# Performance work log

Hardware: AMD Instinct MI355X
Metric: run time of the kernel (lower is better)

The kernel has to match this reference:

```python
import jax, jax.numpy as jnp
import numpy as np
from jax import lax

B, DIM, H, W = 4, 256, 128, 128
KS, LOC, STRIDES_CFG, HEADS = 5, [2, 3], [1, 2], 8
C2 = DIM // 2
GK = HEADS * KS  # per-pixel dynamic kernel channels

def _kernel_map(ks, kstride, kloc):
    # replicates LSAMixer.generate_kernel_map_1d
    axes, strides, start = [0], [1], 1
    for loc, s in zip(kloc, kstride):
        for num in range(0, loc - start):
            axes.append(num * s + axes[-1] + strides[-1])
            strides.append(s)
        start = loc
    patch = (axes[-1] + strides[-1]) * 2 - 1
    full_axes = [-a for a in axes[:0:-1]] + axes
    full_strides = strides[:0:-1] + strides
    return full_axes, full_strides, patch

OFFS, STRDS, PATCH = _kernel_map(KS, STRIDES_CFG, LOC)
PAD = PATCH // 2

def _pw(x, w, b):
    # 1x1 conv as GEMM
    return jnp.einsum('bchw,oc->bohw', x, w) + b[None, :, None, None]

def _dw(x, w, b, ph, pw):
    # depthwise conv, torch OIHW layout with I=1
    y = lax.conv_general_dilated(x, w, (1, 1), [(ph, ph), (pw, pw)],
                                 feature_group_count=x.shape[1],
                                 dimension_numbers=('NCHW', 'OIHW', 'NCHW'))
    return y + b[None, :, None, None]

def _fsa(x, kern, groups, axis):
    # dynamic local attention: for each tap k (offset a, stride s) gather the
    # average of x over the s-wide strided window along `axis`, weight it by
    # the per-head dynamic kernel, and accumulate.
    Bx, Cx, Hx, Wx = x.shape
    gd = Cx // groups
    K = len(OFFS)
    L = x.shape[axis]
    padcfg = [(0, 0)] * 4
    padcfg[axis] = (PAD, PAD)
    xp = jnp.pad(x, padcfg)
    taps = []
    for a, s in zip(OFFS, STRDS):
        start = a if a >= 0 else a - s + 1  # window covers s pixels away from center
        acc = lax.slice_in_dim(xp, PAD + start, PAD + start + L, axis=axis)
        for d in range(1, s):
            acc = acc + lax.slice_in_dim(xp, PAD + start + d, PAD + start + d + L, axis=axis)
        taps.append(acc / s)
    t = jnp.stack(taps, 0).reshape(K, Bx, groups, gd, Hx, Wx)
    k = kern.reshape(Bx, groups, K, Hx, Wx)
    return jnp.einsum('kbgdhw,bgkhw->bgdhw', t, k).reshape(Bx, Cx, Hx, Wx)

def setup_inputs() -> dict:
    key = jax.random.key(0)
    ks = jax.random.split(key, 12)
    sc = 0.02
    f32 = jnp.float32
    return {
        'x': jax.random.normal(ks[0], (B, DIM, H, W), f32),
        'proj_in_w': jax.random.normal(ks[1], (DIM, DIM), f32) * sc,
        'proj_in_b': jnp.zeros((DIM,), f32),
        'hk_dw_w': jax.random.normal(ks[2], (C2, 1, 1, PATCH), f32) * sc,
        'hk_dw_b': jnp.zeros((C2,), f32),
        'hk_pw_w': jax.random.normal(ks[3], (GK, C2), f32) * sc,
        'hk_pw_b': jnp.zeros((GK,), f32),
        'vk_dw_w': jax.random.normal(ks[4], (C2, 1, PATCH, 1), f32) * sc,
        'vk_dw_b': jnp.zeros((C2,), f32),
        'vk_pw_w': jax.random.normal(ks[5], (GK, C2), f32) * sc,
        'vk_pw_b': jnp.zeros((GK,), f32),
        'cb_w1': jax.random.normal(ks[6], (DIM // 4, C2), f32) * sc,
        'cb_b1': jnp.zeros((DIM // 4,), f32),
        'cb_w2': jax.random.normal(ks[7], (C2, DIM // 4), f32) * sc,
        'cb_b2': jnp.zeros((C2,), f32),
        'proj_out_w': jax.random.normal(ks[8], (DIM, DIM), f32) * sc,
        'proj_out_b': jnp.zeros((DIM,), f32),
    }

def reference(x, proj_in_w, proj_in_b, hk_dw_w, hk_dw_b, hk_pw_w, hk_pw_b,
              vk_dw_w, vk_dw_b, vk_pw_w, vk_pw_b, cb_w1, cb_b1, cb_w2, cb_b2,
              proj_out_w, proj_out_b):
    Bv, _, Hv, Wv = x.shape
    h = _pw(x, proj_in_w, proj_in_b)
    x1, x2 = h[:, :C2], h[:, C2:]
    # channel branch: pw -> relu -> pw
    x_conv = _pw(jax.nn.relu(_pw(x1, cb_w1, cb_b1)), cb_w2, cb_b2)
    # horizontal dynamic kernel + fsa
    kh = jnp.tanh(_pw(_dw(x2, hk_dw_w, hk_dw_b, 0, PAD), hk_pw_w, hk_pw_b))
    attn_h = _fsa(x2, kh, HEADS, axis=3)
    # vertical dynamic kernel + fsa
    kv = jnp.tanh(_pw(_dw(attn_h, vk_dw_w, vk_dw_b, PAD, 0), vk_pw_w, vk_pw_b))
    attn = _fsa(attn_h, kv, HEADS, axis=2)
    N = Hv * Wv
    xc = x_conv.reshape(Bv, C2, N)
    at = attn.reshape(Bv, C2, N)
    # SpatialInteraction(x_conv, attn): modulates x_conv
    s_sig = jax.nn.sigmoid(jnp.einsum('bc,bcn->bn', at.mean(-1), xc) / C2)[:, None, :]
    spatial_map = (s_sig * xc).reshape(Bv, C2, Hv, Wv)
    # ChannelInteraction(x_conv, attn): modulates attn
    c_sig = jax.nn.sigmoid(jnp.einsum('bcn,bn->bc', at, xc.mean(1)) / N)[:, :, None]
    channel_map = (c_sig * at).reshape(Bv, C2, Hv, Wv)
    out = jnp.concatenate([spatial_map, channel_map], axis=1)
    return _pw(out, proj_out_w, proj_out_b)
```

## Files before the change

kernel.cpp:

```cpp
#include <hip/hip_runtime.h>
#include <hip/hip_bf16.h>
#include <math.h>

typedef __hip_bfloat16 bf16;
typedef __attribute__((ext_vector_type(8))) short short8;
typedef __attribute__((ext_vector_type(4))) float floatx4;
#define DEV __device__ __forceinline__

constexpr int BATCH = 4;
constexpr int DIM   = 256;
constexpr int C2    = 128;
constexpr int GK    = 40;
constexpr int HH    = 128;
constexpr int WW    = 128;
constexpr int NPIX  = HH * WW;
constexpr int TPB   = 256;

DEV float toF(float v) { return v; }
DEV float toF(bf16 v)  { return __bfloat162float(v); }

DEV unsigned short f2bs(float f) {
  union { bf16 h; unsigned short u; } cv;
  cv.h = __float2bfloat16(f);
  return cv.u;
}
DEV float bs2f(unsigned short u) {
  union { float f; unsigned x; } c;
  c.x = ((unsigned)u) << 16;
  return c.f;
}

template<int N>
DEV void load_f32v(const float* __restrict__ p, float* v) {
  if constexpr (N == 8) {
    const float4 a = *(const float4*)p;
    const float4 b = *(const float4*)(p + 4);
    v[0]=a.x; v[1]=a.y; v[2]=a.z; v[3]=a.w; v[4]=b.x; v[5]=b.y; v[6]=b.z; v[7]=b.w;
  } else if constexpr (N == 4) {
    const float4 a = *(const float4*)p;
    v[0]=a.x; v[1]=a.y; v[2]=a.z; v[3]=a.w;
  } else {
    const float2 a = *(const float2*)p;
    v[0]=a.x; v[1]=a.y;
  }
}
template<int N>
DEV void load_bf16v(const bf16* __restrict__ p, float* v) {
  if constexpr (N == 8) {
    const uint4 u = *(const uint4*)p;
    v[0]=bs2f(u.x & 0xffff); v[1]=bs2f(u.x >> 16);
    v[2]=bs2f(u.y & 0xffff); v[3]=bs2f(u.y >> 16);
    v[4]=bs2f(u.z & 0xffff); v[5]=bs2f(u.z >> 16);
    v[6]=bs2f(u.w & 0xffff); v[7]=bs2f(u.w >> 16);
  } else if constexpr (N == 4) {
    const uint2 u = *(const uint2*)p;
    v[0]=bs2f(u.x & 0xffff); v[1]=bs2f(u.x >> 16);
    v[2]=bs2f(u.y & 0xffff); v[3]=bs2f(u.y >> 16);
  } else {
    const unsigned u = *(const unsigned*)p;
    v[0]=bs2f(u & 0xffff); v[1]=bs2f(u >> 16);
  }
}
DEV void load8bf(const bf16* __restrict__ p, float* v) { load_bf16v<8>(p, v); }

__global__ __launch_bounds__(TPB) void prepack_kernel(
    const float* __restrict__ w0, const float* __restrict__ w1,
    const float* __restrict__ w2, const float* __restrict__ w3,
    const float* __restrict__ w4, const float* __restrict__ w5,
    short* __restrict__ dst) {
  const int i = blockIdx.x * TPB + threadIdx.x;
  if (i >= 157696) return;
  int j = i;
  float v;
  if (j < 65536) v = w0[j];
  else if ((j -= 65536) < 8192) v = w1[j];
  else if ((j -= 8192) < 8192) v = w2[j];
  else if ((j -= 8192) < 5120) v = w3[j];
  else if ((j -= 5120) < 5120) v = w4[j];
  else { j -= 5120; v = w5[j]; }
  dst[i] = (short)f2bs(v);
}

template<int K, int O, int ACT, int GATED, typename TIN, typename TOUT>
__global__ __launch_bounds__(TPB) void pw2_kernel(
    const TIN* __restrict__ in, int in_bs,
    const short* __restrict__ wbf, const float* __restrict__ bias,
    TOUT* __restrict__ out, int out_bs,
    const bf16* __restrict__ gxc, const bf16* __restrict__ gattn,
    const float* __restrict__ gs, const float* __restrict__ gc) {
  constexpr int C8   = K / 8;
  constexpr int PXT  = K / 32;
  constexpr int PG   = 64 / PXT;
  constexpr int ROWB = K * 2 + 16;
  constexpr int WO   = (O + 63) / 64;
  __shared__ char smem[64 * ROWB];

  const int p0   = blockIdx.x * 64;
  const int b    = blockIdx.y;
  const int t    = threadIdx.x;
  const int lane = t & 63, wid = t >> 6;
  const int q    = lane >> 4, i16 = lane & 15;

  {
    const int c8  = t / PG;
    const int px0 = (t % PG) * PXT;
    float vals[8][PXT];
    float svals[PXT];
    if constexpr (GATED) {
      if (c8 < C8 / 2) load_f32v<PXT>(gs + (size_t)b * NPIX + p0 + px0, svals);
    }
#pragma unroll
    for (int j = 0; j < 8; ++j) {
      const int c = c8 * 8 + j;
      float tmp[PXT];
      if constexpr (GATED) {
        if (c < C2) {
          load_bf16v<PXT>(gxc + ((size_t)b * C2 + c) * NPIX + p0 + px0, tmp);
#pragma unroll
          for (int px = 0; px < PXT; ++px) vals[j][px] = tmp[px] * svals[px];
        } else {
          const float cg = gc[b * C2 + (c - C2)];
          load_bf16v<PXT>(gattn + ((size_t)b * C2 + (c - C2)) * NPIX + p0 + px0, tmp);
#pragma unroll
          for (int px = 0; px < PXT; ++px) vals[j][px] = tmp[px] * cg;
        }
      } else {
        const TIN* src = in + ((size_t)b * in_bs + c) * NPIX + p0 + px0;
        if constexpr (sizeof(TIN) == 4) load_f32v<PXT>((const float*)src, tmp);
        else                            load_bf16v<PXT>((const bf16*)src, tmp);
#pragma unroll
        for (int px = 0; px < PXT; ++px) vals[j][px] = tmp[px];
      }
    }
#pragma unroll
    for (int px = 0; px < PXT; ++px) {
      const int p = px0 + px;
      short8 pk;
#pragma unroll
      for (int j = 0; j < 8; ++j) pk[j] = (short)f2bs(vals[j][px]);
      const int phys = c8 ^ ((p >> 3) & 7);
      *reinterpret_cast<short8*>(smem + (size_t)p * ROWB + phys * 16) = pk;
    }
  }
  __syncthreads();

  const int o_base = wid * WO * 16;
  if (o_base >= O) return;

  floatx4 acc[WO][4];
#pragma unroll
  for (int ot = 0; ot < WO; ++ot)
#pragma unroll
    for (int nt = 0; nt < 4; ++nt)
      acc[ot][nt] = (floatx4){0.f, 0.f, 0.f, 0.f};

  for (int kc = 0; kc < K / 32; ++kc) {
    short8 afrag[WO];
#pragma unroll
    for (int ot = 0; ot < WO; ++ot) {
      int o = o_base + ot * 16 + i16;
      if (o >= O) o = O - 1;
      afrag[ot] = *reinterpret_cast<const short8*>(wbf + (size_t)o * K + kc * 32 + q * 8);
    }
    short8 bfrag[4];
#pragma unroll
    for (int nt = 0; nt < 4; ++nt) {
      const int n = nt * 16 + i16;
      const int phys = (kc * 4 + q) ^ ((n >> 3) & 7);
      bfrag[nt] = *reinterpret_cast<const short8*>(smem + (size_t)n * ROWB + phys * 16);
    }
#pragma unroll
    for (int ot = 0; ot < WO; ++ot)
#pragma unroll
      for (int nt = 0; nt < 4; ++nt)
        acc[ot][nt] = __builtin_amdgcn_mfma_f32_16x16x32_bf16(
            afrag[ot], bfrag[nt], acc[ot][nt], 0, 0, 0);
  }

#pragma unroll
  for (int ot = 0; ot < WO; ++ot) {
#pragma unroll
    for (int reg = 0; reg < 4; ++reg) {
      const int o = o_base + ot * 16 + q * 4 + reg;
      if (o < O) {
        const float bv = bias[o];
#pragma unroll
        for (int nt = 0; nt < 4; ++nt) {
          float v = acc[ot][nt][reg] + bv;
          if (ACT == 1) v = fmaxf(v, 0.0f);
          if (ACT == 2) v = tanhf(v);
          TOUT* dst = out + ((size_t)b * out_bs + o) * NPIX + p0 + nt * 16 + i16;
          if constexpr (sizeof(TOUT) == 4) *dst = v;
          else *dst = __float2bfloat16(v);
        }
      }
    }
  }
}

__global__ __launch_bounds__(TPB) void pwfused_kernel(
    const float* __restrict__ x,
    const short* __restrict__ w_pi, const float* __restrict__ pib,
    const short* __restrict__ w_cb1, const float* __restrict__ cbb1,
    const short* __restrict__ w_cb2, const float* __restrict__ cbb2,
    float* __restrict__ x2out, bf16* __restrict__ xconv) {
  constexpr int ROWB  = 256 * 2 + 16;
  constexpr int HROWB = 128 * 2 + 16;
  constexpr int TROWB = 64 * 2 + 16;
  __shared__ char smem[64 * ROWB];
  __shared__ char hbuf[64 * HROWB];
  __shared__ char tbuf[64 * TROWB];

  const int p0   = blockIdx.x * 64;
  const int b    = blockIdx.y;
  const int t    = threadIdx.x;
  const int lane = t & 63, wid = t >> 6;
  const int q    = lane >> 4, i16 = lane & 15;

  {
    const int c8  = t / 8;
    const int px0 = (t % 8) * 8;
    float vals[8][8];
#pragma unroll
    for (int j = 0; j < 8; ++j) {
      const int c = c8 * 8 + j;
      load_f32v<8>(x + ((size_t)b * DIM + c) * NPIX + p0 + px0, vals[j]);
    }
#pragma unroll
    for (int px = 0; px < 8; ++px) {
      const int p = px0 + px;
      short8 pk;
#pragma unroll
      for (int j = 0; j < 8; ++j) pk[j] = (short)f2bs(vals[j][px]);
      const int phys = c8 ^ ((p >> 3) & 7);
      *reinterpret_cast<short8*>(smem + (size_t)p * ROWB + phys * 16) = pk;
    }
  }
  __syncthreads();

  const int o_base = wid * 64;
  {
    floatx4 acc[4][4];
#pragma unroll
    for (int ot = 0; ot < 4; ++ot)
#pragma unroll
      for (int nt = 0; nt < 4; ++nt)
        acc[ot][nt] = (floatx4){0.f, 0.f, 0.f, 0.f};

    for (int kc = 0; kc < 8; ++kc) {
      short8 afrag[4];
#pragma unroll
      for (int ot = 0; ot < 4; ++ot) {
        const int o = o_base + ot * 16 + i16;
        afrag[ot] = *reinterpret_cast<const short8*>(w_pi + (size_t)o * 256 + kc * 32 + q * 8);
      }
      short8 bfrag[4];
#pragma unroll
      for (int nt = 0; nt < 4; ++nt) {
        const int n = nt * 16 + i16;
        const int phys = (kc * 4 + q) ^ ((n >> 3) & 7);
        bfrag[nt] = *reinterpret_cast<const short8*>(smem + (size_t)n * ROWB + phys * 16);
      }
#pragma unroll
      for (int ot = 0; ot < 4; ++ot)
#pragma unroll
        for (int nt = 0; nt < 4; ++nt)
          acc[ot][nt] = __builtin_amdgcn_mfma_f32_16x16x32_bf16(
              afrag[ot], bfrag[nt], acc[ot][nt], 0, 0, 0);
    }

#pragma unroll
    for (int ot = 0; ot < 4; ++ot) {
      const int ch0 = o_base + ot * 16 + q * 4;
      if (ch0 >= C2) {
#pragma unroll
        for (int reg = 0; reg < 4; ++reg) {
          const int o = ch0 + reg;
          const float bv = pib[o];
#pragma unroll
          for (int nt = 0; nt < 4; ++nt)
            x2out[((size_t)b * C2 + (o - C2)) * NPIX + p0 + nt * 16 + i16] =
                acc[ot][nt][reg] + bv;
        }
      } else {
        float bv4[4];
#pragma unroll
        for (int reg = 0; reg < 4; ++reg) bv4[reg] = pib[ch0 + reg];
#pragma unroll
        for (int nt = 0; nt < 4; ++nt) {
          const int px = nt * 16 + i16;
          ushort4 pk;
          pk.x = f2bs(acc[ot][nt][0] + bv4[0]);
          pk.y = f2bs(acc[ot][nt][1] + bv4[1]);
          pk.z = f2bs(acc[ot][nt][2] + bv4[2]);
          pk.w = f2bs(acc[ot][nt][3] + bv4[3]);
          const int phys = (ch0 >> 3) ^ ((px >> 3) & 7);
          *reinterpret_cast<ushort4*>(hbuf + (size_t)px * HROWB + phys * 16 +
                                      (ch0 & 7) * 2) = pk;
        }
      }
    }
  }
  __syncthreads();

  {
    floatx4 acc2[4];
#pragma unroll
    for (int nt = 0; nt < 4; ++nt) acc2[nt] = (floatx4){0.f, 0.f, 0.f, 0.f};
    const int o2b = wid * 16;
    for (int kc = 0; kc < 4; ++kc) {
      const short8 afrag = *reinterpret_cast<const short8*>(
          w_cb1 + (size_t)(o2b + i16) * 128 + kc * 32 + q * 8);
      short8 bfrag[4];
#pragma unroll
      for (int nt = 0; nt < 4; ++nt) {
        const int n = nt * 16 + i16;
        const int phys = (kc * 4 + q) ^ ((n >> 3) & 7);
        bfrag[nt] = *reinterpret_cast<const short8*>(hbuf + (size_t)n * HROWB + phys * 16);
      }
#pragma unroll
      for (int nt = 0; nt < 4; ++nt)
        acc2[nt] = __builtin_amdgcn_mfma_f32_16x16x32_bf16(afrag, bfrag[nt], acc2[nt], 0, 0, 0);
    }
    const int ch0 = o2b + q * 4;
    float bv4[4];
#pragma unroll
    for (int reg = 0; reg < 4; ++reg) bv4[reg] = cbb1[ch0 + reg];
#pragma unroll
    for (int nt = 0; nt < 4; ++nt) {
      const int px = nt * 16 + i16;
      ushort4 pk;
      pk.x = f2bs(fmaxf(acc2[nt][0] + bv4[0], 0.f));
      pk.y = f2bs(fmaxf(acc2[nt][1] + bv4[1], 0.f));
      pk.z = f2bs(fmaxf(acc2[nt][2] + bv4[2], 0.f));
      pk.w = f2bs(fmaxf(acc2[nt][3] + bv4[3], 0.f));
      const int phys = (ch0 >> 3) ^ ((px >> 3) & 7);
      *reinterpret_cast<ushort4*>(tbuf + (size_t)px * TROWB + phys * 16 +
                                  (ch0 & 7) * 2) = pk;
    }
  }
  __syncthreads();

  {
    floatx4 acc3[2][4];
#pragma unroll
    for (int ot = 0; ot < 2; ++ot)
#pragma unroll
      for (int nt = 0; nt < 4; ++nt) acc3[ot][nt] = (floatx4){0.f, 0.f, 0.f, 0.f};
    const int o3b = wid * 32;
    for (int kc = 0; kc < 2; ++kc) {
      short8 afrag[2];
#pragma unroll
      for (int ot = 0; ot < 2; ++ot)
        afrag[ot] = *reinterpret_cast<const short8*>(
            w_cb2 + (size_t)(o3b + ot * 16 + i16) * 64 + kc * 32 + q * 8);
      short8 bfrag[4];
#pragma unroll
      for (int nt = 0; nt < 4; ++nt) {
        const int n = nt * 16 + i16;
        const int phys = (kc * 4 + q) ^ ((n >> 3) & 7);
        bfrag[nt] = *reinterpret_cast<const short8*>(tbuf + (size_t)n * TROWB + phys * 16);
      }
#pragma unroll
      for (int ot = 0; ot < 2; ++ot)
#pragma unroll
        for (int nt = 0; nt < 4; ++nt)
          acc3[ot][nt] = __builtin_amdgcn_mfma_f32_16x16x32_bf16(
              afrag[ot], bfrag[nt], acc3[ot][nt], 0, 0, 0);
    }
#pragma unroll
    for (int ot = 0; ot < 2; ++ot) {
#pragma unroll
      for (int reg = 0; reg < 4; ++reg) {
        const int o = o3b + ot * 16 + q * 4 + reg;
        const float bv = cbb2[o];
#pragma unroll
        for (int nt = 0; nt < 4; ++nt)
          xconv[((size_t)b * C2 + o) * NPIX + p0 + nt * 16 + i16] =
              __float2bfloat16(acc3[ot][nt][reg] + bv);
      }
    }
  }
}

__global__ __launch_bounds__(TPB) void dwh2_kernel(
    const float* __restrict__ in, int in_bs,
    const float* __restrict__ w7, const float* __restrict__ bias,
    bf16* __restrict__ out) {
  const int g  = blockIdx.x * TPB + threadIdx.x;
  const int w8 = g & 15;
  const int hp = (g >> 4) & (HH - 1);
  const int c  = (g >> 11) & (C2 - 1);
  const int b  = g >> 18;
  const float* xr = in + ((size_t)b * in_bs + c) * NPIX + hp * WW;
  const int px0 = w8 * 8;
  float xs[14];
  if (w8 > 0) { const float4 L = *(const float4*)(xr + px0 - 4); xs[0]=L.y; xs[1]=L.z; xs[2]=L.w; }
  else { xs[0]=xs[1]=xs[2]=0.f; }
  { const float4 a = *(const float4*)(xr + px0);
    const float4 bq = *(const float4*)(xr + px0 + 4);
    xs[3]=a.x; xs[4]=a.y; xs[5]=a.z; xs[6]=a.w;
    xs[7]=bq.x; xs[8]=bq.y; xs[9]=bq.z; xs[10]=bq.w; }
  if (w8 < 15) { const float4 R = *(const float4*)(xr + px0 + 8); xs[11]=R.x; xs[12]=R.y; xs[13]=R.z; }
  else { xs[11]=xs[12]=xs[13]=0.f; }
  float wv[7];
#pragma unroll
  for (int j = 0; j < 7; ++j) wv[j] = w7[c * 7 + j];
  const float bv = bias[c];
  short8 o;
#pragma unroll
  for (int i = 0; i < 8; ++i) {
    float a = bv;
#pragma unroll
    for (int j = 0; j < 7; ++j) a = fmaf(wv[j], xs[i + j], a);
    o[i] = (short)f2bs(a);
  }
  *reinterpret_cast<short8*>(out + ((size_t)(b * C2 + c)) * NPIX + hp * WW + px0) = o;
}

__global__ __launch_bounds__(TPB) void dwv2_kernel(
    const bf16* __restrict__ in,
    const float* __restrict__ w7, const float* __restrict__ bias,
    bf16* __restrict__ out) {
  const int g  = blockIdx.x * TPB + threadIdx.x;
  const int w8 = g & 15;
  const int hp = (g >> 4) & (HH - 1);
  const int c  = (g >> 11) & (C2 - 1);
  const int b  = g >> 18;
  const int px0 = w8 * 8;
  const bf16* base = in + ((size_t)(b * C2 + c)) * NPIX + px0;
  float r[7][8];
#pragma unroll
  for (int j = 0; j < 7; ++j) {
    const int hq = hp - 3 + j;
    if (hq >= 0 && hq < HH) load8bf(base + (size_t)hq * WW, r[j]);
    else
#pragma unroll
      for (int i = 0; i < 8; ++i) r[j][i] = 0.f;
  }
  float wv[7];
#pragma unroll
  for (int j = 0; j < 7; ++j) wv[j] = w7[c * 7 + j];
  const float bv = bias[c];
  short8 o;
#pragma unroll
  for (int i = 0; i < 8; ++i) {
    float a = bv;
#pragma unroll
    for (int j = 0; j < 7; ++j) a = fmaf(wv[j], r[j][i], a);
    o[i] = (short)f2bs(a);
  }
  *reinterpret_cast<short8*>(out + ((size_t)(b * C2 + c)) * NPIX + hp * WW + px0) = o;
}

__global__ __launch_bounds__(TPB) void fsah2_kernel(
    const float* __restrict__ x, int x_bs,
    const bf16* __restrict__ kern, bf16* __restrict__ out) {
  const int g  = blockIdx.x * TPB + threadIdx.x;
  const int w8 = g & 15;
  const int hp = (g >> 4) & (HH - 1);
  const int c  = (g >> 11) & (C2 - 1);
  const int b  = g >> 18;
  const float* xr = x + ((size_t)b * x_bs + c) * NPIX + hp * WW;
  const int px0 = w8 * 8;
  float xs[14];
  if (w8 > 0) { const float4 L = *(const float4*)(xr + px0 - 4); xs[0]=L.y; xs[1]=L.z; xs[2]=L.w; }
  else { xs[0]=xs[1]=xs[2]=0.f; }
  { const float4 a = *(const float4*)(xr + px0);
    const float4 bq = *(const float4*)(xr + px0 + 4);
    xs[3]=a.x; xs[4]=a.y; xs[5]=a.z; xs[6]=a.w;
    xs[7]=bq.x; xs[8]=bq.y; xs[9]=bq.z; xs[10]=bq.w; }
  if (w8 < 15) { const float4 R = *(const float4*)(xr + px0 + 8); xs[11]=R.x; xs[12]=R.y; xs[13]=R.z; }
  else { xs[11]=xs[12]=xs[13]=0.f; }
  float k[5][8];
  const bf16* kr = kern + ((size_t)b * GK + (c >> 4) * 5) * NPIX + hp * WW + px0;
#pragma unroll
  for (int tp = 0; tp < 5; ++tp) load8bf(kr + (size_t)tp * NPIX, k[tp]);
  short8 o;
#pragma unroll
  for (int i = 0; i < 8; ++i) {
    float a = 0.5f * (xs[i] + xs[i + 1]) * k[0][i];
    a = fmaf(xs[i + 2], k[1][i], a);
    a = fmaf(xs[i + 3], k[2][i], a);
    a = fmaf(xs[i + 4], k[3][i], a);
    a = fmaf(0.5f * (xs[i + 5] + xs[i + 6]), k[4][i], a);
    o[i] = (short)f2bs(a);
  }
  *reinterpret_cast<short8*>(out + ((size_t)(b * C2 + c)) * NPIX + hp * WW + px0) = o;
}

__global__ __launch_bounds__(TPB) void fsav2_kernel(
    const bf16* __restrict__ x,
    const bf16* __restrict__ kern, bf16* __restrict__ out) {
  const int g  = blockIdx.x * TPB + threadIdx.x;
  const int w8 = g & 15;
  const int hp = (g >> 4) & (HH - 1);
  const int c  = (g >> 11) & (C2 - 1);
  const int b  = g >> 18;
  const int px0 = w8 * 8;
  const bf16* base = x + ((size_t)(b * C2 + c)) * NPIX + px0;
  float r[7][8];
#pragma unroll
  for (int j = 0; j < 7; ++j) {
    const int hq = hp - 3 + j;
    if (hq >= 0 && hq < HH) load8bf(base + (size_t)hq * WW, r[j]);
    else
#pragma unroll
      for (int i = 0; i < 8; ++i) r[j][i] = 0.f;
  }
  float k[5][8];
  const bf16* kr = kern + ((size_t)b * GK + (c >> 4) * 5) * NPIX + hp * WW + px0;
#pragma unroll
  for (int tp = 0; tp < 5; ++tp) load8bf(kr + (size_t)tp * NPIX, k[tp]);
  short8 o;
#pragma unroll
  for (int i = 0; i < 8; ++i) {
    float a = 0.5f * (r[0][i] + r[1][i]) * k[0][i];
    a = fmaf(r[2][i], k[1][i], a);
    a = fmaf(r[3][i], k[2][i], a);
    a = fmaf(r[4][i], k[3][i], a);
    a = fmaf(0.5f * (r[5][i] + r[6][i]), k[4][i], a);
    o[i] = (short)f2bs(a);
  }
  *reinterpret_cast<short8*>(out + ((size_t)(b * C2 + c)) * NPIX + hp * WW + px0) = o;
}

DEV float block_reduce_sum(float v) {
#pragma unroll
  for (int off = 32; off > 0; off >>= 1) v += __shfl_down(v, off, 64);
  __shared__ float ls[TPB / 64];
  const int lane = threadIdx.x & 63;
  const int wid  = threadIdx.x >> 6;
  if (lane == 0) ls[wid] = v;
  __syncthreads();
  float s = 0.0f;
  if (threadIdx.x == 0) {
#pragma unroll
    for (int i = 0; i < TPB / 64; ++i) s += ls[i];
  }
  return s;
}

__global__ __launch_bounds__(TPB) void mean_n_kernel(const bf16* __restrict__ in,
                                                     float* __restrict__ out) {
  const int bc = blockIdx.x;
  const bf16* r = in + (size_t)bc * NPIX;
  float s = 0.0f;
  for (int i = threadIdx.x * 8; i < NPIX; i += TPB * 8) {
    float v[8];
    load8bf(r + i, v);
#pragma unroll
    for (int j = 0; j < 8; ++j) s += v[j];
  }
  s = block_reduce_sum(s);
  if (threadIdx.x == 0) out[bc] = s * (1.0f / NPIX);
}

__global__ __launch_bounds__(TPB) void xs_kernel(const bf16* __restrict__ xc,
                                                 const float* __restrict__ at_mean,
                                                 float* __restrict__ xc_mean,
                                                 float* __restrict__ s_sig) {
  __shared__ float am[C2];
  const int b = blockIdx.y;
  if (threadIdx.x < C2) am[threadIdx.x] = at_mean[b * C2 + threadIdx.x];
  __syncthreads();
  const int p = blockIdx.x * TPB + threadIdx.x;
  const bf16* r = xc + (size_t)b * C2 * NPIX + p;
  float s = 0.0f, m = 0.0f;
#pragma unroll 4
  for (int c = 0; c < C2; ++c) {
    const float v = toF(r[(size_t)c * NPIX]);
    m += v;
    s = fmaf(am[c], v, s);
  }
  xc_mean[(size_t)b * NPIX + p] = m * (1.0f / C2);
  s_sig[(size_t)b * NPIX + p]   = 1.0f / (1.0f + expf(-s * (1.0f / C2)));
}

__global__ __launch_bounds__(TPB) void csig_kernel(const bf16* __restrict__ attn,
                                                   const float* __restrict__ xc_mean,
                                                   float* __restrict__ out) {
  const int bc = blockIdx.x;
  const int b  = bc / C2;
  const bf16* r = attn + (size_t)bc * NPIX;
  const float* m = xc_mean + (size_t)b * NPIX;
  float s = 0.0f;
  for (int i = threadIdx.x * 8; i < NPIX; i += TPB * 8) {
    float v[8], mm[8];
    load8bf(r + i, v);
    load_f32v<8>(m + i, mm);
#pragma unroll
    for (int j = 0; j < 8; ++j) s = fmaf(v[j], mm[j], s);
  }
  s = block_reduce_sum(s);
  if (threadIdx.x == 0) out[bc] = 1.0f / (1.0f + expf(-s * (1.0f / NPIX)));
}

extern "C" void kernel_launch(void* const* d_in, const int* in_sizes, int n_in,
                              void* d_out, int out_size, void* d_ws, size_t ws_size,
                              hipStream_t stream) {
  const float* x    = (const float*)d_in[0];
  const float* piw  = (const float*)d_in[1];
  const float* pib  = (const float*)d_in[2];
  const float* hkdw = (const float*)d_in[3];
  const float* hkdb = (const float*)d_in[4];
  const float* hkpw = (const float*)d_in[5];
  const float* hkpb = (const float*)d_in[6];
  const float* vkdw = (const float*)d_in[7];
  const float* vkdb = (const float*)d_in[8];
  const float* vkpw = (const float*)d_in[9];
  const float* vkpb = (const float*)d_in[10];
  const float* cbw1 = (const float*)d_in[11];
  const float* cbb1 = (const float*)d_in[12];
  const float* cbw2 = (const float*)d_in[13];
  const float* cbb2 = (const float*)d_in[14];
  const float* pow_ = (const float*)d_in[15];
  const float* pob  = (const float*)d_in[16];
  float* out = (float*)d_out;

  char* ws = (char*)d_ws;
  size_t off = 0;
  auto alloc = [&](size_t bytes) -> char* {
    char* p = ws + off;
    off += (bytes + 255) & ~(size_t)255;
    return p;
  };
  short* wpk    = (short*)alloc(157696 * 2);
  float* x2buf  = (float*)alloc((size_t)BATCH * C2  * NPIX * 4);
  bf16*  x_conv = (bf16*) alloc((size_t)BATCH * C2  * NPIX * 2);
  bf16*  dwbuf  = (bf16*) alloc((size_t)BATCH * C2  * NPIX * 2);
  bf16*  kbuf   = (bf16*) alloc((size_t)BATCH * GK  * NPIX * 2);
  bf16*  attn_h = (bf16*) alloc((size_t)BATCH * C2  * NPIX * 2);
  bf16*  attn   = (bf16*) alloc((size_t)BATCH * C2  * NPIX * 2);
  float* at_mean = (float*)alloc((size_t)BATCH * C2 * 4);
  float* xc_mean = (float*)alloc((size_t)BATCH * NPIX * 4);
  float* s_sig   = (float*)alloc((size_t)BATCH * NPIX * 4);
  float* c_sig   = (float*)alloc((size_t)BATCH * C2 * 4);

  const short* w_pi  = wpk;
  const short* w_cb1 = wpk + 65536;
  const short* w_cb2 = wpk + 73728;
  const short* w_hk  = wpk + 81920;
  const short* w_vk  = wpk + 87040;
  const short* w_po  = wpk + 92160;

  const dim3 blk(TPB);
  const dim3 gemm_grid(NPIX / 64, BATCH);
  const int PT  = NPIX / TPB;
  const int EL8 = BATCH * C2 * HH * 16 / TPB;

  prepack_kernel<<<dim3((157696 + TPB - 1) / TPB), blk, 0, stream>>>(
      piw, cbw1, cbw2, hkpw, vkpw, pow_, wpk);
  pwfused_kernel<<<gemm_grid, blk, 0, stream>>>(
      x, w_pi, pib, w_cb1, cbb1, w_cb2, cbb2, x2buf, x_conv);
  dwh2_kernel<<<dim3(EL8), blk, 0, stream>>>(x2buf, C2, hkdw, hkdb, dwbuf);
  pw2_kernel<128, 40, 2, 0, bf16, bf16><<<gemm_grid, blk, 0, stream>>>(
      dwbuf, C2, w_hk, hkpb, kbuf, GK, nullptr, nullptr, nullptr, nullptr);
  fsah2_kernel<<<dim3(EL8), blk, 0, stream>>>(x2buf, C2, kbuf, attn_h);
  dwv2_kernel<<<dim3(EL8), blk, 0, stream>>>(attn_h, vkdw, vkdb, dwbuf);
  pw2_kernel<128, 40, 2, 0, bf16, bf16><<<gemm_grid, blk, 0, stream>>>(
      dwbuf, C2, w_vk, vkpb, kbuf, GK, nullptr, nullptr, nullptr, nullptr);
  fsav2_kernel<<<dim3(EL8), blk, 0, stream>>>(attn_h, kbuf, attn);
  mean_n_kernel<<<dim3(BATCH * C2), blk, 0, stream>>>(attn, at_mean);
  xs_kernel<<<dim3(PT, BATCH), blk, 0, stream>>>(x_conv, at_mean, xc_mean, s_sig);
  csig_kernel<<<dim3(BATCH * C2), blk, 0, stream>>>(attn, xc_mean, c_sig);
  pw2_kernel<256, 256, 0, 1, bf16, float><<<gemm_grid, blk, 0, stream>>>(
      x_conv, 0, w_po, pob, out, DIM, x_conv, attn, s_sig, c_sig);
}
```

Before: 283.9 us.

## Fuse depthwise convs into pointwise GEMM staging and fold mean into fsav

The horizontal and vertical 7-tap depthwise convolutions now run inside the staging phase of the pointwise kernel-generation GEMM, which removes the dwh2/dwv2 kernels and the bf16 dwbuf round trip through memory. The attention mean is now taken inside fsav2 through a block reduction and an atomicAdd into a zeroed buffer, with the 1/NPIX scale applied in xs_kernel, which removes mean_n_kernel. The cost is redundant halo loads, since each 4-pixel group rereads its neighbours (up to 7 rows for the vertical conv), and atomic ordering that makes the mean sum nondeterministic.

```diff
diff --git a/kernel.cpp b/kernel.cpp
--- a/kernel.cpp
+++ b/kernel.cpp
@@ -81,18 +81,20 @@
   dst[i] = (short)f2bs(v);
 }
 
-template<int K, int O, int ACT, int GATED, typename TIN, typename TOUT>
+template<int K, int O, int ACT, int GATED, int DW, typename TIN, typename TOUT>
 __global__ __launch_bounds__(TPB) void pw2_kernel(
     const TIN* __restrict__ in, int in_bs,
     const short* __restrict__ wbf, const float* __restrict__ bias,
     TOUT* __restrict__ out, int out_bs,
     const bf16* __restrict__ gxc, const bf16* __restrict__ gattn,
-    const float* __restrict__ gs, const float* __restrict__ gc) {
+    const float* __restrict__ gs, const float* __restrict__ gc,
+    const float* __restrict__ dww, const float* __restrict__ dwb) {
   constexpr int C8   = K / 8;
   constexpr int PXT  = K / 32;
   constexpr int PG   = 64 / PXT;
   constexpr int ROWB = K * 2 + 16;
   constexpr int WO   = (O + 63) / 64;
+  static_assert(DW == 0 || PXT == 4, "DW fusion assumes K=128 staging shape");
   __shared__ char smem[64 * ROWB];
 
   const int p0   = blockIdx.x * 64;
@@ -105,31 +107,86 @@
     const int c8  = t / PG;
     const int px0 = (t % PG) * PXT;
     float vals[8][PXT];
-    float svals[PXT];
-    if constexpr (GATED) {
-      if (c8 < C8 / 2) load_f32v<PXT>(gs + (size_t)b * NPIX + p0 + px0, svals);
-    }
-#pragma unroll
-    for (int j = 0; j < 8; ++j) {
-      const int c = c8 * 8 + j;
-      float tmp[PXT];
+    if constexpr (DW == 1) {
+      const int p = p0 + px0;
+      const int row = p >> 7, w0 = p & (WW - 1);
+#pragma unroll
+      for (int j = 0; j < 8; ++j) {
+        const int c = c8 * 8 + j;
+        const float* xr = (const float*)in + ((size_t)b * C2 + c) * NPIX + row * WW;
+        float xs[10];
+        if (w0 > 0) { const float4 L = *(const float4*)(xr + w0 - 4); xs[0]=L.y; xs[1]=L.z; xs[2]=L.w; }
+        else { xs[0]=xs[1]=xs[2]=0.f; }
+        { const float4 A = *(const float4*)(xr + w0); xs[3]=A.x; xs[4]=A.y; xs[5]=A.z; xs[6]=A.w; }
+        if (w0 < WW - 4) { const float4 R = *(const float4*)(xr + w0 + 4); xs[7]=R.x; xs[8]=R.y; xs[9]=R.z; }
+        else { xs[7]=xs[8]=xs[9]=0.f; }
+        float wv[7];
+#pragma unroll
+        for (int k = 0; k < 7; ++k) wv[k] = dww[c * 7 + k];
+        const float bv = dwb[c];
+#pragma unroll
+        for (int px = 0; px < PXT; ++px) {
+          float a = bv;
+#pragma unroll
+          for (int k = 0; k < 7; ++k) a = fmaf(wv[k], xs[px + k], a);
+          vals[j][px] = a;
+        }
+      }
+    } else if constexpr (DW == 2) {
+      const int p = p0 + px0;
+      const int row = p >> 7, w0 = p & (WW - 1);
+#pragma unroll
+      for (int j = 0; j < 8; ++j) {
+        const int c = c8 * 8 + j;
+        const bf16* base = (const bf16*)in + ((size_t)b * C2 + c) * NPIX + w0;
+        float rr[7][PXT];
+#pragma unroll
+        for (int k = 0; k < 7; ++k) {
+          const int hq = row - 3 + k;
+          if (hq >= 0 && hq < HH) load_bf16v<PXT>(base + (size_t)hq * WW, rr[k]);
+          else
+#pragma unroll
+            for (int px = 0; px < PXT; ++px) rr[k][px] = 0.f;
+        }
+        float wv[7];
+#pragma unroll
+        for (int k = 0; k < 7; ++k) wv[k] = dww[c * 7 + k];
+        const float bv = dwb[c];
+#pragma unroll
+        for (int px = 0; px < PXT; ++px) {
+          float a = bv;
+#pragma unroll
+          for (int k = 0; k < 7; ++k) a = fmaf(wv[k], rr[k][px], a);
+          vals[j][px] = a;
+        }
+      }
+    } else {
+      float svals[PXT];
       if constexpr (GATED) {
-        if (c < C2) {
-          load_bf16v<PXT>(gxc + ((size_t)b * C2 + c) * NPIX + p0 + px0, tmp);
-#pragma unroll
-          for (int px = 0; px < PXT; ++px) vals[j][px] = tmp[px] * svals[px];
+        if (c8 < C8 / 2) load_f32v<PXT>(gs + (size_t)b * NPIX + p0 + px0, svals);
+      }
+#pragma unroll
+      for (int j = 0; j < 8; ++j) {
+        const int c = c8 * 8 + j;
+        float tmp[PXT];
+        if constexpr (GATED) {
+          if (c < C2) {
+            load_bf16v<PXT>(gxc + ((size_t)b * C2 + c) * NPIX + p0 + px0, tmp);
+#pragma unroll
+            for (int px = 0; px < PXT; ++px) vals[j][px] = tmp[px] * svals[px];
+          } else {
+            const float cg = gc[b * C2 + (c - C2)];
+            load_bf16v<PXT>(gattn + ((size_t)b * C2 + (c - C2)) * NPIX + p0 + px0, tmp);
+#pragma unroll
+            for (int px = 0; px < PXT; ++px) vals[j][px] = tmp[px] * cg;
+          }
         } else {
-          const float cg = gc[b * C2 + (c - C2)];
-          load_bf16v<PXT>(gattn + ((size_t)b * C2 + (c - C2)) * NPIX + p0 + px0, tmp);
-#pragma unroll
-          for (int px = 0; px < PXT; ++px) vals[j][px] = tmp[px] * cg;
+          const TIN* src = in + ((size_t)b * in_bs + c) * NPIX + p0 + px0;
+          if constexpr (sizeof(TIN) == 4) load_f32v<PXT>((const float*)src, tmp);
+          else                            load_bf16v<PXT>((const bf16*)src, tmp);
+#pragma unroll
+          for (int px = 0; px < PXT; ++px) vals[j][px] = tmp[px];
         }
-      } else {
-        const TIN* src = in + ((size_t)b * in_bs + c) * NPIX + p0 + px0;
-        if constexpr (sizeof(TIN) == 4) load_f32v<PXT>((const float*)src, tmp);
-        else                            load_bf16v<PXT>((const bf16*)src, tmp);
-#pragma unroll
-        for (int px = 0; px < PXT; ++px) vals[j][px] = tmp[px];
       }
     }
 #pragma unroll
@@ -383,74 +440,20 @@
   }
 }
 
-__global__ __launch_bounds__(TPB) void dwh2_kernel(
-    const float* __restrict__ in, int in_bs,
-    const float* __restrict__ w7, const float* __restrict__ bias,
-    bf16* __restrict__ out) {
-  const int g  = blockIdx.x * TPB + threadIdx.x;
-  const int w8 = g & 15;
-  const int hp = (g >> 4) & (HH - 1);
-  const int c  = (g >> 11) & (C2 - 1);
-  const int b  = g >> 18;
-  const float* xr = in + ((size_t)b * in_bs + c) * NPIX + hp * WW;
-  const int px0 = w8 * 8;
-  float xs[14];
-  if (w8 > 0) { const float4 L = *(const float4*)(xr + px0 - 4); xs[0]=L.y; xs[1]=L.z; xs[2]=L.w; }
-  else { xs[0]=xs[1]=xs[2]=0.f; }
-  { const float4 a = *(const float4*)(xr + px0);
-    const float4 bq = *(const float4*)(xr + px0 + 4);
-    xs[3]=a.x; xs[4]=a.y; xs[5]=a.z; xs[6]=a.w;
-    xs[7]=bq.x; xs[8]=bq.y; xs[9]=bq.z; xs[10]=bq.w; }
-  if (w8 < 15) { const float4 R = *(const float4*)(xr + px0 + 8); xs[11]=R.x; xs[12]=R.y; xs[13]=R.z; }
-  else { xs[11]=xs[12]=xs[13]=0.f; }
-  float wv[7];
-#pragma unroll
-  for (int j = 0; j < 7; ++j) wv[j] = w7[c * 7 + j];
-  const float bv = bias[c];
-  short8 o;
-#pragma unroll
-  for (int i = 0; i < 8; ++i) {
-    float a = bv;
-#pragma unroll
-    for (int j = 0; j < 7; ++j) a = fmaf(wv[j], xs[i + j], a);
-    o[i] = (short)f2bs(a);
-  }
-  *reinterpret_cast<short8*>(out + ((size_t)(b * C2 + c)) * NPIX + hp * WW + px0) = o;
-}
-
-__global__ __launch_bounds__(TPB) void dwv2_kernel(
-    const bf16* __restrict__ in,
-    const float* __restrict__ w7, const float* __restrict__ bias,
-    bf16* __restrict__ out) {
-  const int g  = blockIdx.x * TPB + threadIdx.x;
-  const int w8 = g & 15;
-  const int hp = (g >> 4) & (HH - 1);
-  const int c  = (g >> 11) & (C2 - 1);
-  const int b  = g >> 18;
-  const int px0 = w8 * 8;
-  const bf16* base = in + ((size_t)(b * C2 + c)) * NPIX + px0;
-  float r[7][8];
-#pragma unroll
-  for (int j = 0; j < 7; ++j) {
-    const int hq = hp - 3 + j;
-    if (hq >= 0 && hq < HH) load8bf(base + (size_t)hq * WW, r[j]);
-    else
-#pragma unroll
-      for (int i = 0; i < 8; ++i) r[j][i] = 0.f;
-  }
-  float wv[7];
-#pragma unroll
-  for (int j = 0; j < 7; ++j) wv[j] = w7[c * 7 + j];
-  const float bv = bias[c];
-  short8 o;
-#pragma unroll
-  for (int i = 0; i < 8; ++i) {
-    float a = bv;
-#pragma unroll
-    for (int j = 0; j < 7; ++j) a = fmaf(wv[j], r[j][i], a);
-    o[i] = (short)f2bs(a);
-  }
-  *reinterpret_cast<short8*>(out + ((size_t)(b * C2 + c)) * NPIX + hp * WW + px0) = o;
+DEV float block_reduce_sum(float v) {
+#pragma unroll
+  for (int off = 32; off > 0; off >>= 1) v += __shfl_down(v, off, 64);
+  __shared__ float ls[TPB / 64];
+  const int lane = threadIdx.x & 63;
+  const int wid  = threadIdx.x >> 6;
+  if (lane == 0) ls[wid] = v;
+  __syncthreads();
+  float s = 0.0f;
+  if (threadIdx.x == 0) {
+#pragma unroll
+    for (int i = 0; i < TPB / 64; ++i) s += ls[i];
+  }
+  return s;
 }
 
 __global__ __launch_bounds__(TPB) void fsah2_kernel(
@@ -491,7 +494,8 @@
 
 __global__ __launch_bounds__(TPB) void fsav2_kernel(
     const bf16* __restrict__ x,
-    const bf16* __restrict__ kern, bf16* __restrict__ out) {
+    const bf16* __restrict__ kern, bf16* __restrict__ out,
+    float* __restrict__ at_mean) {
   const int g  = blockIdx.x * TPB + threadIdx.x;
   const int w8 = g & 15;
   const int hp = (g >> 4) & (HH - 1);
@@ -513,6 +517,7 @@
 #pragma unroll
   for (int tp = 0; tp < 5; ++tp) load8bf(kr + (size_t)tp * NPIX, k[tp]);
   short8 o;
+  float ps = 0.0f;
 #pragma unroll
   for (int i = 0; i < 8; ++i) {
     float a = 0.5f * (r[0][i] + r[1][i]) * k[0][i];
@@ -521,39 +526,11 @@
     a = fmaf(r[4][i], k[3][i], a);
     a = fmaf(0.5f * (r[5][i] + r[6][i]), k[4][i], a);
     o[i] = (short)f2bs(a);
+    ps += bs2f((unsigned short)o[i]);
   }
   *reinterpret_cast<short8*>(out + ((size_t)(b * C2 + c)) * NPIX + hp * WW + px0) = o;
-}
-
-DEV float block_reduce_sum(float v) {
-#pragma unroll
-  for (int off = 32; off > 0; off >>= 1) v += __shfl_down(v, off, 64);
-  __shared__ float ls[TPB / 64];
-  const int lane = threadIdx.x & 63;
-  const int wid  = threadIdx.x >> 6;
-  if (lane == 0) ls[wid] = v;
-  __syncthreads();
-  float s = 0.0f;
-  if (threadIdx.x == 0) {
-#pragma unroll
-    for (int i = 0; i < TPB / 64; ++i) s += ls[i];
-  }
-  return s;
-}
-
-__global__ __launch_bounds__(TPB) void mean_n_kernel(const bf16* __restrict__ in,
-                                                     float* __restrict__ out) {
-  const int bc = blockIdx.x;
-  const bf16* r = in + (size_t)bc * NPIX;
-  float s = 0.0f;
-  for (int i = threadIdx.x * 8; i < NPIX; i += TPB * 8) {
-    float v[8];
-    load8bf(r + i, v);
-#pragma unroll
-    for (int j = 0; j < 8; ++j) s += v[j];
-  }
-  s = block_reduce_sum(s);
-  if (threadIdx.x == 0) out[bc] = s * (1.0f / NPIX);
+  const float s = block_reduce_sum(ps);
+  if (threadIdx.x == 0) atomicAdd(&at_mean[b * C2 + c], s);
 }
 
 __global__ __launch_bounds__(TPB) void xs_kernel(const bf16* __restrict__ xc,
@@ -562,7 +539,7 @@
                                                  float* __restrict__ s_sig) {
   __shared__ float am[C2];
   const int b = blockIdx.y;
-  if (threadIdx.x < C2) am[threadIdx.x] = at_mean[b * C2 + threadIdx.x];
+  if (threadIdx.x < C2) am[threadIdx.x] = at_mean[b * C2 + threadIdx.x] * (1.0f / NPIX);
   __syncthreads();
   const int p = blockIdx.x * TPB + threadIdx.x;
   const bf16* r = xc + (size_t)b * C2 * NPIX + p;
@@ -628,7 +605,6 @@
   short* wpk    = (short*)alloc(157696 * 2);
   float* x2buf  = (float*)alloc((size_t)BATCH * C2  * NPIX * 4);
   bf16*  x_conv = (bf16*) alloc((size_t)BATCH * C2  * NPIX * 2);
-  bf16*  dwbuf  = (bf16*) alloc((size_t)BATCH * C2  * NPIX * 2);
   bf16*  kbuf   = (bf16*) alloc((size_t)BATCH * GK  * NPIX * 2);
   bf16*  attn_h = (bf16*) alloc((size_t)BATCH * C2  * NPIX * 2);
   bf16*  attn   = (bf16*) alloc((size_t)BATCH * C2  * NPIX * 2);
@@ -651,19 +627,17 @@
 
   prepack_kernel<<<dim3((157696 + TPB - 1) / TPB), blk, 0, stream>>>(
       piw, cbw1, cbw2, hkpw, vkpw, pow_, wpk);
+  hipMemsetAsync(at_mean, 0, (size_t)BATCH * C2 * 4, stream);
   pwfused_kernel<<<gemm_grid, blk, 0, stream>>>(
       x, w_pi, pib, w_cb1, cbb1, w_cb2, cbb2, x2buf, x_conv);
-  dwh2_kernel<<<dim3(EL8), blk, 0, stream>>>(x2buf, C2, hkdw, hkdb, dwbuf);
-  pw2_kernel<128, 40, 2, 0, bf16, bf16><<<gemm_grid, blk, 0, stream>>>(
-      dwbuf, C2, w_hk, hkpb, kbuf, GK, nullptr, nullptr, nullptr, nullptr);
+  pw2_kernel<128, 40, 2, 0, 1, float, bf16><<<gemm_grid, blk, 0, stream>>>(
+      x2buf, C2, w_hk, hkpb, kbuf, GK, nullptr, nullptr, nullptr, nullptr, hkdw, hkdb);
   fsah2_kernel<<<dim3(EL8), blk, 0, stream>>>(x2buf, C2, kbuf, attn_h);
-  dwv2_kernel<<<dim3(EL8), blk, 0, stream>>>(attn_h, vkdw, vkdb, dwbuf);
-  pw2_kernel<128, 40, 2, 0, bf16, bf16><<<gemm_grid, blk, 0, stream>>>(
-      dwbuf, C2, w_vk, vkpb, kbuf, GK, nullptr, nullptr, nullptr, nullptr);
-  fsav2_kernel<<<dim3(EL8), blk, 0, stream>>>(attn_h, kbuf, attn);
-  mean_n_kernel<<<dim3(BATCH * C2), blk, 0, stream>>>(attn, at_mean);
+  pw2_kernel<128, 40, 2, 0, 2, bf16, bf16><<<gemm_grid, blk, 0, stream>>>(
+      attn_h, C2, w_vk, vkpb, kbuf, GK, nullptr, nullptr, nullptr, nullptr, vkdw, vkdb);
+  fsav2_kernel<<<dim3(EL8), blk, 0, stream>>>(attn_h, kbuf, attn, at_mean);
   xs_kernel<<<dim3(PT, BATCH), blk, 0, stream>>>(x_conv, at_mean, xc_mean, s_sig);
   csig_kernel<<<dim3(BATCH * C2), blk, 0, stream>>>(attn, xc_mean, c_sig);
-  pw2_kernel<256, 256, 0, 1, bf16, float><<<gemm_grid, blk, 0, stream>>>(
-      x_conv, 0, w_po, pob, out, DIM, x_conv, attn, s_sig, c_sig);
-}
+  pw2_kernel<256, 256, 0, 1, 0, bf16, float><<<gemm_grid, blk, 0, stream>>>(
+      x_conv, 0, w_po, pob, out, DIM, x_conv, attn, s_sig, c_sig, nullptr, nullptr);
+}
```

Result: slower. 346.9 us (+22.2%).
